# Performance work log

Hardware: AMD Instinct MI355X
Metric: run time of the kernel (lower is better)

Reference implementation:

```python
import jax, jax.numpy as jnp
import numpy as np

B, S, H, NH, FF, L = 2, 2048, 768, 12, 3072, 2
DH = H // NH
EPS = 1e-12
NEG = -10000.0


def setup_inputs() -> dict:
    key = jax.random.key(0)
    ks = jax.random.split(key, 10)
    w = lambda k, shp: jax.random.normal(k, shp, dtype=jnp.float32) * 0.02
    return {
        'hidden_states': jax.random.normal(ks[0], (B, S, H), dtype=jnp.float32),
        'attention_mask': jnp.ones((B, S), jnp.float32),
        'bias_matrix': jax.random.normal(ks[1], (S, S), dtype=jnp.float32) * 0.1,
        'bias_coef': jnp.ones((), jnp.float32),
        'Wq': w(ks[2], (L, H, H)), 'bq': jnp.zeros((L, H), jnp.float32),
        'Wk': w(ks[3], (L, H, H)), 'bk': jnp.zeros((L, H), jnp.float32),
        'Wv': w(ks[4], (L, H, H)), 'bv': jnp.zeros((L, H), jnp.float32),
        'Wo': w(ks[5], (L, H, H)), 'bo': jnp.zeros((L, H), jnp.float32),
        'ln1_g': jnp.ones((L, H), jnp.float32), 'ln1_b': jnp.zeros((L, H), jnp.float32),
        'Wi': w(ks[6], (L, H, FF)), 'bi': jnp.zeros((L, FF), jnp.float32),
        'Wo2': w(ks[7], (L, FF, H)), 'bo2': jnp.zeros((L, H), jnp.float32),
        'ln2_g': jnp.ones((L, H), jnp.float32), 'ln2_b': jnp.zeros((L, H), jnp.float32),
    }


def _layer_norm(x, g, b):
    mu = jnp.mean(x, axis=-1, keepdims=True)
    var = jnp.mean(jnp.square(x - mu), axis=-1, keepdims=True)
    return (x - mu) * jax.lax.rsqrt(var + EPS) * g + b


def reference(hidden_states, attention_mask, bias_matrix, bias_coef,
              Wq, bq, Wk, bk, Wv, bv, Wo, bo, ln1_g, ln1_b,
              Wi, bi, Wo2, bo2, ln2_g, ln2_b):
    # extended additive mask: [B,1,1,S]
    ext_mask = (1.0 - attention_mask)[:, None, None, :] * NEG
    bias = bias_matrix[None, None] * bias_coef  # [1,1,S,S]
    x = hidden_states
    scale = 1.0 / np.sqrt(DH)
    for i in range(L):
        q = (x @ Wq[i] + bq[i]).reshape(B, S, NH, DH).transpose(0, 2, 1, 3)
        k = (x @ Wk[i] + bk[i]).reshape(B, S, NH, DH).transpose(0, 2, 1, 3)
        v = (x @ Wv[i] + bv[i]).reshape(B, S, NH, DH).transpose(0, 2, 1, 3)
        scores = jnp.einsum('bhqd,bhkd->bhqk', q, k) * scale
        scores = scores + bias + ext_mask
        probs = jax.nn.softmax(scores, axis=-1)  # dropout = identity (eval)
        ctx = jnp.einsum('bhqk,bhkd->bhqd', probs, v)
        ctx = ctx.transpose(0, 2, 1, 3).reshape(B, S, H)
        attn_out = ctx @ Wo[i] + bo[i]
        x = _layer_norm(attn_out + x, ln1_g[i], ln1_b[i])
        inter = jax.nn.gelu(x @ Wi[i] + bi[i], approximate=False)
        ffn_out = inter @ Wo2[i] + bo2[i]
        x = _layer_norm(ffn_out + x, ln2_g[i], ln2_b[i])
    return x
```

## Files before the change

kernel.cpp:

```cpp
#include <hip/hip_runtime.h>
#include <hip/hip_bf16.h>
#include <math.h>

#define BB     2
#define SS     2048
#define HH     768
#define NHEAD  12
#define DHEAD  64
#define FFD    3072
#define NLAYER 2
#define MTOK   (BB*SS)
#define LOG2E  1.4426950408889634f
#define QSCALE 0.18033688011112042f

typedef __attribute__((ext_vector_type(8))) short bf16x8;
typedef __attribute__((ext_vector_type(4))) short bf16x4;
typedef __attribute__((ext_vector_type(4))) float f32x4;

__device__ __forceinline__ short f2bs(float f) {
    union { float f; unsigned u; } v; v.f = f;
    unsigned r = v.u + 0x7FFF + ((v.u >> 16) & 1);
    return (short)(r >> 16);
}
__device__ __forceinline__ float bs2f(short s) {
    union { unsigned u; float f; } v; v.u = ((unsigned)(unsigned short)s) << 16;
    return v.f;
}
__device__ __forceinline__ void gl2lds16(const short* g, short* l) {
    __builtin_amdgcn_global_load_lds(
        (const __attribute__((address_space(1))) unsigned int*)g,
        (__attribute__((address_space(3))) unsigned int*)l, 16, 0, 0);
}

struct TJobs { const float* src[8]; short* dst[8]; };

__global__ __launch_bounds__(256)
void transpose_cvt_batch(TJobs jobs, int K, int N)
{
    const float* __restrict__ W  = jobs.src[blockIdx.z];
    short* __restrict__ Wt = jobs.dst[blockIdx.z];
    __shared__ short tile[32][33];
    const int k0 = blockIdx.x * 32, n0 = blockIdx.y * 32;
    const int tx = threadIdx.x & 31, ty = threadIdx.x >> 5;
#pragma unroll
    for (int i = 0; i < 4; i++)
        tile[ty + i*8][tx] = f2bs(W[(size_t)(k0 + ty + i*8) * N + n0 + tx]);
    __syncthreads();
#pragma unroll
    for (int i = 0; i < 4; i++)
        Wt[(size_t)(n0 + ty + i*8) * K + k0 + tx] = tile[tx][ty + i*8];
}

__global__ __launch_bounds__(256)
void cvt_bf16(const float* __restrict__ src, short* __restrict__ dst, int n)
{
    const int i = blockIdx.x * 256 + threadIdx.x;
    if (i < n) dst[i] = f2bs(src[i]);
}

__global__ __launch_bounds__(256)
void pack_bias(const float* __restrict__ bq, const float* __restrict__ bk,
               const float* __restrict__ bv, float* __restrict__ bqkv)
{
    const int t = blockIdx.x * 256 + threadIdx.x;
    if (t >= NLAYER * 2304) return;
    const int l = t / 2304, r = t % 2304;
    const float* src = (r < 768) ? bq : (r < 1536 ? bk : bv);
    bqkv[t] = src[l*768 + (r % 768)];
}

__global__ __launch_bounds__(256)
void bias_frag_prep(const float* __restrict__ biasM, const float* __restrict__ mask,
                    const float* __restrict__ coefp, short* __restrict__ bFrag)
{
    __shared__ float tile[64][129];
    const int tid = threadIdx.x;
    const int qb = blockIdx.x, q0 = qb*64, k0 = blockIdx.y*128;
#pragma unroll
    for (int p = 0; p < 8; p++) {
        const int row = p*8 + (tid >> 5);
        const int col = (tid & 31) * 4;
        float4 v = *(const float4*)&biasM[(size_t)(q0 + row)*SS + k0 + col];
        tile[row][col+0] = v.x; tile[row][col+1] = v.y;
        tile[row][col+2] = v.z; tile[row][col+3] = v.w;
    }
    __syncthreads();
    const float coef = coefp[0];
    const int lane = tid & 63, w = tid >> 6;
    const int l16 = lane & 15, g = lane >> 4;
    const int qrow = w*16 + l16;
#pragma unroll
    for (int b = 0; b < BB; b++) {
#pragma unroll
        for (int kt = 0; kt < 8; kt++) {
            bf16x4 o;
#pragma unroll
            for (int r = 0; r < 4; r++) {
                const int kk = kt*16 + g*4 + r;
                const float madd = (1.f - mask[b*SS + k0 + kk]) * (-10000.0f);
                o[r] = f2bs((tile[qrow][kk] * coef + madd) * LOG2E);
            }
            const size_t idx = ((((size_t)b*32 + qb)*4 + w)*128 + (k0>>4) + kt)*256 + lane*4;
            *(bf16x4*)&bFrag[idx] = o;
        }
    }
}

__global__ __launch_bounds__(256)
void gemm_mfma(const short* __restrict__ A, const short* __restrict__ Bt,
               const float* __restrict__ bias, short* __restrict__ C, int ldc,
               int M, int N, int K, int gelu, short* __restrict__ VtOut, int vsplit,
               float qscale, int qcols)
{
    __shared__ short sA[2][128*32];
    __shared__ short sB[2][128*32];
    const int tid  = threadIdx.x;
    const int w    = tid >> 6;
    const int lane = tid & 63;
    const int l16  = lane & 15, g = lane >> 4;
    const int wm   = w & 1, wn = w >> 1;
    const size_t m0 = (size_t)blockIdx.y * 128, n0 = (size_t)blockIdx.x * 128;

    const int srow = lane >> 2;
    const int kc   = lane & 3;

    f32x4 acc[4][4];
#pragma unroll
    for (int i = 0; i < 4; i++)
#pragma unroll
        for (int j = 0; j < 4; j++) acc[i][j] = (f32x4){0.f,0.f,0.f,0.f};

    const short* gA0 = A  + (m0 + w*32 +      srow) * (size_t)K + kc*8;
    const short* gA1 = A  + (m0 + w*32 + 16 + srow) * (size_t)K + kc*8;
    const short* gB0 = Bt + (n0 + w*32 +      srow) * (size_t)K + kc*8;
    const short* gB1 = Bt + (n0 + w*32 + 16 + srow) * (size_t)K + kc*8;
    const int oA0 = (w*32     )*32, oA1 = (w*32 + 16)*32;

    for (int k0 = 0; k0 < K; k0 += 64) {
        gl2lds16(gA0 + k0,      &sA[0][oA0]);
        gl2lds16(gA1 + k0,      &sA[0][oA1]);
        gl2lds16(gB0 + k0,      &sB[0][oA0]);
        gl2lds16(gB1 + k0,      &sB[0][oA1]);
        gl2lds16(gA0 + k0 + 32, &sA[1][oA0]);
        gl2lds16(gA1 + k0 + 32, &sA[1][oA1]);
        gl2lds16(gB0 + k0 + 32, &sB[1][oA0]);
        gl2lds16(gB1 + k0 + 32, &sB[1][oA1]);
        __syncthreads();

#pragma unroll
        for (int s = 0; s < 2; s++) {
            bf16x8 af[4], bfr[4];
#pragma unroll
            for (int mt = 0; mt < 4; mt++)
                af[mt] = *(const bf16x8*)&sA[s][(wm*64 + mt*16 + l16)*32 + g*8];
#pragma unroll
            for (int nt = 0; nt < 4; nt++)
                bfr[nt] = *(const bf16x8*)&sB[s][(wn*64 + nt*16 + l16)*32 + g*8];
#pragma unroll
            for (int mt = 0; mt < 4; mt++)
#pragma unroll
                for (int nt = 0; nt < 4; nt++)
                    acc[mt][nt] = __builtin_amdgcn_mfma_f32_16x16x32_bf16(
                                      af[mt], bfr[nt], acc[mt][nt], 0, 0, 0);
        }
        __syncthreads();
    }

#pragma unroll
    for (int mt = 0; mt < 4; mt++) {
        const size_t row0 = m0 + wm*64 + mt*16 + g*4;
#pragma unroll
        for (int nt = 0; nt < 4; nt++) {
            const size_t col = n0 + wn*64 + nt*16 + l16;
            if ((int)col >= vsplit) {
                short4 t;
                t.x = f2bs(acc[mt][nt][0] + bias[col]);
                t.y = f2bs(acc[mt][nt][1] + bias[col]);
                t.z = f2bs(acc[mt][nt][2] + bias[col]);
                t.w = f2bs(acc[mt][nt][3] + bias[col]);
                *(short4*)&VtOut[(size_t)(col - vsplit)*MTOK + row0] = t;
            } else {
#pragma unroll
                for (int r = 0; r < 4; r++) {
                    float v = acc[mt][nt][r] + bias[col];
                    if ((int)col < qcols) v *= qscale;
                    if (gelu) v = 0.5f * v * (1.f + erff(v * 0.70710678118f));
                    C[(row0 + r) * (size_t)ldc + col] = f2bs(v);
                }
            }
        }
    }
}

__global__ __launch_bounds__(256)
void gemm_n64_splitk(const short* __restrict__ A, const short* __restrict__ Bt,
                     float* __restrict__ P, int K)
{
    const int K2 = K >> 1;
    const int z  = blockIdx.z;
    __shared__ short sA[2][128*32];
    __shared__ short sB[2][64*32];
    const int tid  = threadIdx.x;
    const int w    = tid >> 6;
    const int lane = tid & 63;
    const int l16  = lane & 15, g = lane >> 4;
    const int wm   = w & 1, wn = w >> 1;
    const size_t m0 = (size_t)blockIdx.y * 128, n0 = (size_t)blockIdx.x * 64;

    const int srow = lane >> 2;
    const int kc   = lane & 3;

    f32x4 acc[4][2];
#pragma unroll
    for (int i = 0; i < 4; i++)
#pragma unroll
        for (int j = 0; j < 2; j++) acc[i][j] = (f32x4){0.f,0.f,0.f,0.f};

    const short* gA0 = A  + (m0 + w*32 +      srow) * (size_t)K + z*K2 + kc*8;
    const short* gA1 = A  + (m0 + w*32 + 16 + srow) * (size_t)K + z*K2 + kc*8;
    const short* gB0 = Bt + (n0 + w*16 +      srow) * (size_t)K + z*K2 + kc*8;
    const int oA0 = (w*32     )*32, oA1 = (w*32 + 16)*32, oB0 = (w*16)*32;

    for (int k0 = 0; k0 < K2; k0 += 64) {
        gl2lds16(gA0 + k0,      &sA[0][oA0]);
        gl2lds16(gA1 + k0,      &sA[0][oA1]);
        gl2lds16(gB0 + k0,      &sB[0][oB0]);
        gl2lds16(gA0 + k0 + 32, &sA[1][oA0]);
        gl2lds16(gA1 + k0 + 32, &sA[1][oA1]);
        gl2lds16(gB0 + k0 + 32, &sB[1][oB0]);
        __syncthreads();

#pragma unroll
        for (int s = 0; s < 2; s++) {
            bf16x8 af[4], bfr[2];
#pragma unroll
            for (int mt = 0; mt < 4; mt++)
                af[mt] = *(const bf16x8*)&sA[s][(wm*64 + mt*16 + l16)*32 + g*8];
#pragma unroll
            for (int nt = 0; nt < 2; nt++)
                bfr[nt] = *(const bf16x8*)&sB[s][(wn*32 + nt*16 + l16)*32 + g*8];
#pragma unroll
            for (int mt = 0; mt < 4; mt++)
#pragma unroll
                for (int nt = 0; nt < 2; nt++)
                    acc[mt][nt] = __builtin_amdgcn_mfma_f32_16x16x32_bf16(
                                      af[mt], bfr[nt], acc[mt][nt], 0, 0, 0);
        }
        __syncthreads();
    }

    float* Pz = P + (size_t)z * MTOK * HH;
#pragma unroll
    for (int mt = 0; mt < 4; mt++) {
        const size_t row0 = m0 + wm*64 + mt*16 + g*4;
#pragma unroll
        for (int nt = 0; nt < 2; nt++) {
            const size_t col = n0 + wn*32 + nt*16 + l16;
#pragma unroll
            for (int r = 0; r < 4; r++)
                Pz[(row0 + r) * (size_t)HH + col] = acc[mt][nt][r];
        }
    }
}

__global__ __launch_bounds__(256, 3)
void attn_fused(const short* __restrict__ QK, const short* __restrict__ Vt,
                const short* __restrict__ bFrag, short* __restrict__ CTX)
{
    __shared__ short sK[128*72];
    __shared__ short sV[64*136];

    const int qb  = blockIdx.x;
    const int q0  = qb * 64;
    const int h   = blockIdx.y;
    const int b   = blockIdx.z;
    const int tid = threadIdx.x;
    const int w   = tid >> 6;
    const int lane = tid & 63;
    const int l16 = lane & 15;
    const int g   = lane >> 4;

    const short* qrow = QK + ((size_t)(b*SS) + q0 + w*16 + l16) * 1536 + h*64;
    bf16x8 bQ0 = *(const bf16x8*)(qrow + g*8);
    bf16x8 bQ1 = *(const bf16x8*)(qrow + 32 + g*8);

    f32x4 O[4];
#pragma unroll
    for (int d = 0; d < 4; d++) O[d] = (f32x4){0.f,0.f,0.f,0.f};
    float m_q = -1e30f, l_q = 0.f;

    const int krow = tid >> 3, kch = tid & 7;
    const int vrow = tid >> 4, vch = tid & 15;
    const short* Kg = QK + ((size_t)(b*SS) + krow)*1536 + 768 + h*64 + kch*8;
    const short* Vg = Vt + ((size_t)(h*64 + vrow))*MTOK + b*SS + vch*8;
    const short* bF = bFrag + ((((size_t)b*32 + qb)*4 + w)*128)*256 + lane*4;

    bf16x8 kreg[4], vreg[4];
#pragma unroll
    for (int p = 0; p < 4; p++) {
        kreg[p] = *(const bf16x8*)(Kg + (size_t)(p*32)*1536);
        vreg[p] = *(const bf16x8*)(Vg + (size_t)(p*16)*MTOK);
    }

    for (int k0 = 0; k0 < SS; k0 += 128) {
        const short* bFt = bF + ((size_t)(k0 >> 4))*256;
        bf16x4 bb[8];
#pragma unroll
        for (int t = 0; t < 8; t++)
            bb[t] = *(const bf16x4*)(bFt + (size_t)t*256);

#pragma unroll
        for (int p = 0; p < 4; p++) {
            *(bf16x8*)&sK[(p*32 + krow)*72 + kch*8]   = kreg[p];
            *(bf16x8*)&sV[(p*16 + vrow)*136 + vch*8]  = vreg[p];
        }
        __syncthreads();

        if (k0 + 128 < SS) {
#pragma unroll
            for (int p = 0; p < 4; p++) {
                kreg[p] = *(const bf16x8*)(Kg + (size_t)(k0 + 128 + p*32)*1536);
                vreg[p] = *(const bf16x8*)(Vg + (size_t)(p*16)*MTOK + k0 + 128);
            }
        }

        float S[8][4];
#pragma unroll
        for (int t = 0; t < 8; t++) {
            bf16x8 aK0 = *(const bf16x8*)&sK[(t*16 + l16)*72 + g*8];
            bf16x8 aK1 = *(const bf16x8*)&sK[(t*16 + l16)*72 + 32 + g*8];
            f32x4 c = (f32x4){0.f,0.f,0.f,0.f};
            c = __builtin_amdgcn_mfma_f32_16x16x32_bf16(aK0, bQ0, c, 0, 0, 0);
            c = __builtin_amdgcn_mfma_f32_16x16x32_bf16(aK1, bQ1, c, 0, 0, 0);
#pragma unroll
            for (int r = 0; r < 4; r++)
                S[t][r] = c[r] + bs2f(bb[t][r]);
        }

        float tm[8];
#pragma unroll
        for (int t = 0; t < 8; t++)
            tm[t] = fmaxf(fmaxf(S[t][0], S[t][1]), fmaxf(S[t][2], S[t][3]));
        float mx = fmaxf(fmaxf(fmaxf(tm[0], tm[1]), fmaxf(tm[2], tm[3])),
                         fmaxf(fmaxf(tm[4], tm[5]), fmaxf(tm[6], tm[7])));
        mx = fmaxf(mx, __shfl_xor(mx, 16));
        mx = fmaxf(mx, __shfl_xor(mx, 32));
        const float mnew  = fmaxf(m_q, mx);
        const float alpha = exp2f(m_q - mnew);
        float ts[8];
#pragma unroll
        for (int t = 0; t < 8; t++) {
            float p0 = exp2f(S[t][0] - mnew);
            float p1 = exp2f(S[t][1] - mnew);
            float p2 = exp2f(S[t][2] - mnew);
            float p3 = exp2f(S[t][3] - mnew);
            S[t][0] = p0; S[t][1] = p1; S[t][2] = p2; S[t][3] = p3;
            ts[t] = (p0 + p1) + (p2 + p3);
        }
        float rs = ((ts[0] + ts[1]) + (ts[2] + ts[3]))
                 + ((ts[4] + ts[5]) + (ts[6] + ts[7]));
        rs += __shfl_xor(rs, 16);
        rs += __shfl_xor(rs, 32);
        l_q = l_q * alpha + rs;
        m_q = mnew;

#pragma unroll
        for (int r = 0; r < 4; r++) {
            const float ar = __shfl(alpha, g*4 + r);
#pragma unroll
            for (int d = 0; d < 4; d++) O[d][r] *= ar;
        }

#define PVU(u)                                                                 \
        {                                                                      \
            unsigned pa, pb, pc, pe;                                           \
            asm("v_cvt_pk_bf16_f32 %0, %1, %2" : "=v"(pa)                      \
                : "v"(S[2*(u)][0]),   "v"(S[2*(u)][1]));                       \
            asm("v_cvt_pk_bf16_f32 %0, %1, %2" : "=v"(pb)                      \
                : "v"(S[2*(u)][2]),   "v"(S[2*(u)][3]));                       \
            asm("v_cvt_pk_bf16_f32 %0, %1, %2" : "=v"(pc)                      \
                : "v"(S[2*(u)+1][0]), "v"(S[2*(u)+1][1]));                     \
            asm("v_cvt_pk_bf16_f32 %0, %1, %2" : "=v"(pe)                      \
                : "v"(S[2*(u)+1][2]), "v"(S[2*(u)+1][3]));                     \
            asm("v_permlane32_swap_b32 %0, %1" : "+v"(pa), "+v"(pc));          \
            asm("v_permlane16_swap_b32 %0, %1" : "+v"(pa), "+v"(pc));          \
            asm("v_permlane32_swap_b32 %0, %1" : "+v"(pb), "+v"(pe));          \
            asm("v_permlane16_swap_b32 %0, %1" : "+v"(pb), "+v"(pe));          \
            union { unsigned uw[4]; bf16x8 v; } P_;                            \
            P_.uw[0] = pa; P_.uw[1] = pb; P_.uw[2] = pc; P_.uw[3] = pe;        \
            _Pragma("unroll")                                                  \
            for (int d = 0; d < 4; d++) {                                      \
                bf16x8 vv = *(const bf16x8*)&sV[(d*16 + l16)*136 + (u)*32 + g*8]; \
                O[d] = __builtin_amdgcn_mfma_f32_16x16x32_bf16(                \
                           P_.v, vv, O[d], 0, 0, 0);                           \
            }                                                                  \
        }
        PVU(0)
        PVU(1)
        PVU(2)
        PVU(3)
#undef PVU

        __syncthreads();
    }

    float linv[4];
#pragma unroll
    for (int r = 0; r < 4; r++)
        linv[r] = 1.f / __shfl(l_q, g*4 + r);
#pragma unroll
    for (int d = 0; d < 4; d++)
#pragma unroll
        for (int r = 0; r < 4; r++)
            CTX[((size_t)(b*SS) + q0 + w*16 + g*4 + r)*HH + h*64 + d*16 + l16]
                = f2bs(O[d][r] * linv[r]);
}

__global__ __launch_bounds__(256)
void add_ln3(const float* __restrict__ P, const float* __restrict__ bvec,
             const short* __restrict__ R,
             const float* __restrict__ g, const float* __restrict__ beta,
             short* __restrict__ Out, float* __restrict__ OutF)
{
    const int lane = threadIdx.x & 63;
    const int row  = blockIdx.x * 4 + (threadIdx.x >> 6);
    const size_t base = (size_t)row * HH;
    const size_t sH = (size_t)MTOK * HH;

    float v[12];
    float s = 0.f;
#pragma unroll
    for (int p = 0; p < 3; p++) {
        const int c = p*256 + lane*4;
        float4 p0 = *(const float4*)&P[base + c];
        float4 p1 = *(const float4*)&P[sH + base + c];
        float4 bv4 = *(const float4*)&bvec[c];
        bf16x4 rv = *(const bf16x4*)&R[base + c];
        float x0 = p0.x + p1.x + bv4.x + bs2f(rv[0]);
        float x1 = p0.y + p1.y + bv4.y + bs2f(rv[1]);
        float x2 = p0.z + p1.z + bv4.z + bs2f(rv[2]);
        float x3 = p0.w + p1.w + bv4.w + bs2f(rv[3]);
        v[p*4+0] = x0; v[p*4+1] = x1; v[p*4+2] = x2; v[p*4+3] = x3;
        s += (x0 + x1) + (x2 + x3);
    }
    s += __shfl_xor(s, 1);  s += __shfl_xor(s, 2);  s += __shfl_xor(s, 4);
    s += __shfl_xor(s, 8);  s += __shfl_xor(s, 16); s += __shfl_xor(s, 32);
    const float mu = s * (1.f / HH);

    float s2 = 0.f;
#pragma unroll
    for (int j = 0; j < 12; j++) { float d = v[j] - mu; s2 += d * d; }
    s2 += __shfl_xor(s2, 1);  s2 += __shfl_xor(s2, 2);  s2 += __shfl_xor(s2, 4);
    s2 += __shfl_xor(s2, 8);  s2 += __shfl_xor(s2, 16); s2 += __shfl_xor(s2, 32);
    const float rstd = rsqrtf(s2 * (1.f / HH) + 1e-12f);

#pragma unroll
    for (int p = 0; p < 3; p++) {
        const int c = p*256 + lane*4;
        float4 gv = *(const float4*)&g[c];
        float4 bv = *(const float4*)&beta[c];
        float o0 = (v[p*4+0] - mu) * rstd * gv.x + bv.x;
        float o1 = (v[p*4+1] - mu) * rstd * gv.y + bv.y;
        float o2 = (v[p*4+2] - mu) * rstd * gv.z + bv.z;
        float o3 = (v[p*4+3] - mu) * rstd * gv.w + bv.w;
        bf16x4 ov; ov[0] = f2bs(o0); ov[1] = f2bs(o1); ov[2] = f2bs(o2); ov[3] = f2bs(o3);
        *(bf16x4*)&Out[base + c] = ov;
        if (OutF) {
            float4 of; of.x = o0; of.y = o1; of.z = o2; of.w = o3;
            *(float4*)&OutF[base + c] = of;
        }
    }
}

extern "C" void kernel_launch(void* const* d_in, const int* in_sizes, int n_in,
                              void* d_out, int out_size, void* d_ws, size_t ws_size,
                              hipStream_t stream)
{
    const float* hs    = (const float*)d_in[0];
    const float* mask  = (const float*)d_in[1];
    const float* biasM = (const float*)d_in[2];
    const float* coef  = (const float*)d_in[3];
    const float* Wq    = (const float*)d_in[4];
    const float* bq    = (const float*)d_in[5];
    const float* Wk    = (const float*)d_in[6];
    const float* bk    = (const float*)d_in[7];
    const float* Wv    = (const float*)d_in[8];
    const float* bv    = (const float*)d_in[9];
    const float* Wo    = (const float*)d_in[10];
    const float* bo    = (const float*)d_in[11];
    const float* ln1g  = (const float*)d_in[12];
    const float* ln1b  = (const float*)d_in[13];
    const float* Wi    = (const float*)d_in[14];
    const float* bi    = (const float*)d_in[15];
    const float* Wo2   = (const float*)d_in[16];
    const float* bo2   = (const float*)d_in[17];
    const float* ln2g  = (const float*)d_in[18];
    const float* ln2b  = (const float*)d_in[19];

    const size_t sH   = (size_t)MTOK * HH;
    const size_t sQK  = (size_t)MTOK * 1536;
    const size_t sVt  = (size_t)HH * MTOK;
    const size_t WPL  = 7077888;
    short* wt    = (short*)d_ws;
    float* bqkv  = (float*)(wt + 2*WPL);
    short* bFrag = (short*)(bqkv + 2*2304);
    short* X     = bFrag + (size_t)2*SS*SS;
    short* X2    = X  + sH;
    short* QK    = X2 + sH;
    short* Vt    = QK + sQK;
    short* CTX   = Vt + sVt;
    float* PK    = (float*)(CTX + sH);
    short* INTER = QK;

    const dim3 blk(256);

    TJobs jH, jI, jO;
    for (int l = 0; l < NLAYER; l++) {
        short* wl = wt + (size_t)l * WPL;
        jH.src[l*4+0] = Wq + (size_t)l*HH*HH;  jH.dst[l*4+0] = wl;
        jH.src[l*4+1] = Wk + (size_t)l*HH*HH;  jH.dst[l*4+1] = wl + 768*768;
        jH.src[l*4+2] = Wv + (size_t)l*HH*HH;  jH.dst[l*4+2] = wl + 1536*768;
        jH.src[l*4+3] = Wo + (size_t)l*HH*HH;  jH.dst[l*4+3] = wl + 1769472;
        jI.src[l] = Wi  + (size_t)l*HH*FFD;    jI.dst[l] = wl + 2359296;
        jO.src[l] = Wo2 + (size_t)l*FFD*HH;    jO.dst[l] = wl + 4718592;
    }
    transpose_cvt_batch<<<dim3(24,24,8), blk, 0, stream>>>(jH, HH, HH);
    transpose_cvt_batch<<<dim3(24,96,2), blk, 0, stream>>>(jI, HH, FFD);
    transpose_cvt_batch<<<dim3(96,24,2), blk, 0, stream>>>(jO, FFD, HH);
    bias_frag_prep<<<dim3(SS/64, SS/128), blk, 0, stream>>>(biasM, mask, coef, bFrag);
    pack_bias<<<dim3((NLAYER*2304 + 255)/256), blk, 0, stream>>>(bq, bk, bv, bqkv);
    cvt_bf16<<<dim3((int)((sH + 255)/256)), blk, 0, stream>>>(hs, X, (int)sH);

    const dim3 gQKV(2304/128, MTOK/128);
    const dim3 gSK (HH/64,    MTOK/128, 2);
    const dim3 gFF (FFD/128,  MTOK/128);
    const dim3 gA  (SS/64, NHEAD, BB);
    const dim3 gLN (MTOK/4);
    const int NOSPLIT = 1 << 30;

    for (int l = 0; l < NLAYER; l++) {
        short* wl = wt + (size_t)l * WPL;
        gemm_mfma<<<gQKV, blk, 0, stream>>>(X, wl, bqkv + l*2304, QK, 1536,
                                            MTOK, 2304, HH, 0, Vt, 1536,
                                            QSCALE, 768);
        attn_fused<<<gA, blk, 0, stream>>>(QK, Vt, bFrag, CTX);
        gemm_n64_splitk<<<gSK, blk, 0, stream>>>(CTX, wl + 1769472, PK, HH);
        add_ln3<<<gLN, blk, 0, stream>>>(PK, bo + l*HH, X, ln1g + l*HH, ln1b + l*HH,
                                         X2, nullptr);
        gemm_mfma<<<gFF, blk, 0, stream>>>(X2, wl + 2359296, bi + l*FFD, INTER, FFD,
                                           MTOK, FFD, HH, 1, nullptr, NOSPLIT,
                                           1.f, 0);
        gemm_n64_splitk<<<gSK, blk, 0, stream>>>(INTER, wl + 4718592, PK, FFD);
        add_ln3<<<gLN, blk, 0, stream>>>(PK, bo2 + l*HH, X2, ln2g + l*HH, ln2b + l*HH,
                                         X, (l == NLAYER-1) ? (float*)d_out : nullptr);
    }
}
```

Before: 569.8 us.

## Double-buffer K in LDS, load V fragments straight to registers, use raw v_exp

The attention kernel now keeps two K tiles in LDS so the next tile is written while the current one is consumed, leaving one barrier per iteration. V fragments are no longer staged through LDS: each lane loads its MFMA operand directly from global memory in two halves, ping-ponged so the loads overlap the PV matmuls. exp2f is replaced with the raw v_exp_f32 instruction to drop range-handling code. The aim is less LDS traffic, fewer barriers and better latency hiding, at the cost of more VGPRs (16 extra bf16x8 registers), which could reduce occupancy under launch_bounds(256,3). Global V reads also become less coalesced.

```diff
diff --git a/kernel.cpp b/kernel.cpp
--- a/kernel.cpp
+++ b/kernel.cpp
@@ -26,6 +26,9 @@
     union { unsigned u; float f; } v; v.u = ((unsigned)(unsigned short)s) << 16;
     return v.f;
 }
+__device__ __forceinline__ float fexp2(float x) {
+    float r; asm("v_exp_f32 %0, %1" : "=v"(r) : "v"(x)); return r;
+}
 __device__ __forceinline__ void gl2lds16(const short* g, short* l) {
     __builtin_amdgcn_global_load_lds(
         (const __attribute__((address_space(1))) unsigned int*)g,
@@ -267,8 +270,7 @@
 void attn_fused(const short* __restrict__ QK, const short* __restrict__ Vt,
                 const short* __restrict__ bFrag, short* __restrict__ CTX)
 {
-    __shared__ short sK[128*72];
-    __shared__ short sV[64*136];
+    __shared__ short sK[2][128*72];
 
     const int qb  = blockIdx.x;
     const int q0  = qb * 64;
@@ -290,45 +292,42 @@
     float m_q = -1e30f, l_q = 0.f;
 
     const int krow = tid >> 3, kch = tid & 7;
-    const int vrow = tid >> 4, vch = tid & 15;
     const short* Kg = QK + ((size_t)(b*SS) + krow)*1536 + 768 + h*64 + kch*8;
-    const short* Vg = Vt + ((size_t)(h*64 + vrow))*MTOK + b*SS + vch*8;
+    const short* Vg = Vt + ((size_t)(h*64 + l16))*MTOK + b*SS + g*8;
     const short* bF = bFrag + ((((size_t)b*32 + qb)*4 + w)*128)*256 + lane*4;
 
-    bf16x8 kreg[4], vreg[4];
-#pragma unroll
-    for (int p = 0; p < 4; p++) {
+    bf16x8 kreg[4], vfA[8], vfB[8];
+#pragma unroll
+    for (int p = 0; p < 4; p++)
         kreg[p] = *(const bf16x8*)(Kg + (size_t)(p*32)*1536);
-        vreg[p] = *(const bf16x8*)(Vg + (size_t)(p*16)*MTOK);
-    }
+#pragma unroll
+    for (int p = 0; p < 4; p++)
+        *(bf16x8*)&sK[0][(p*32 + krow)*72 + kch*8] = kreg[p];
+#pragma unroll
+    for (int p = 0; p < 4; p++)
+        kreg[p] = *(const bf16x8*)(Kg + (size_t)(128 + p*32)*1536);
+#pragma unroll
+    for (int u = 0; u < 2; u++)
+#pragma unroll
+        for (int d = 0; d < 4; d++)
+            vfA[u*4+d] = *(const bf16x8*)(Vg + (size_t)(d*16)*MTOK + u*32);
+    __syncthreads();
 
     for (int k0 = 0; k0 < SS; k0 += 128) {
+        const int cur = (k0 >> 7) & 1;
+        const short* sKc = sK[cur];
+
         const short* bFt = bF + ((size_t)(k0 >> 4))*256;
         bf16x4 bb[8];
 #pragma unroll
         for (int t = 0; t < 8; t++)
             bb[t] = *(const bf16x4*)(bFt + (size_t)t*256);
 
-#pragma unroll
-        for (int p = 0; p < 4; p++) {
-            *(bf16x8*)&sK[(p*32 + krow)*72 + kch*8]   = kreg[p];
-            *(bf16x8*)&sV[(p*16 + vrow)*136 + vch*8]  = vreg[p];
-        }
-        __syncthreads();
-
-        if (k0 + 128 < SS) {
-#pragma unroll
-            for (int p = 0; p < 4; p++) {
-                kreg[p] = *(const bf16x8*)(Kg + (size_t)(k0 + 128 + p*32)*1536);
-                vreg[p] = *(const bf16x8*)(Vg + (size_t)(p*16)*MTOK + k0 + 128);
-            }
-        }
-
         float S[8][4];
 #pragma unroll
         for (int t = 0; t < 8; t++) {
-            bf16x8 aK0 = *(const bf16x8*)&sK[(t*16 + l16)*72 + g*8];
-            bf16x8 aK1 = *(const bf16x8*)&sK[(t*16 + l16)*72 + 32 + g*8];
+            bf16x8 aK0 = *(const bf16x8*)&sKc[(t*16 + l16)*72 + g*8];
+            bf16x8 aK1 = *(const bf16x8*)&sKc[(t*16 + l16)*72 + 32 + g*8];
             f32x4 c = (f32x4){0.f,0.f,0.f,0.f};
             c = __builtin_amdgcn_mfma_f32_16x16x32_bf16(aK0, bQ0, c, 0, 0, 0);
             c = __builtin_amdgcn_mfma_f32_16x16x32_bf16(aK1, bQ1, c, 0, 0, 0);
@@ -336,6 +335,24 @@
             for (int r = 0; r < 4; r++)
                 S[t][r] = c[r] + bs2f(bb[t][r]);
         }
+
+        if (k0 + 128 < SS) {
+            short* sKn = sK[cur ^ 1];
+#pragma unroll
+            for (int p = 0; p < 4; p++)
+                *(bf16x8*)&sKn[(p*32 + krow)*72 + kch*8] = kreg[p];
+            if (k0 + 256 < SS) {
+#pragma unroll
+                for (int p = 0; p < 4; p++)
+                    kreg[p] = *(const bf16x8*)(Kg + (size_t)(k0 + 256 + p*32)*1536);
+            }
+        }
+
+#pragma unroll
+        for (int u = 0; u < 2; u++)
+#pragma unroll
+            for (int d = 0; d < 4; d++)
+                vfB[u*4+d] = *(const bf16x8*)(Vg + (size_t)(d*16)*MTOK + k0 + 64 + u*32);
 
         float tm[8];
 #pragma unroll
@@ -346,14 +363,14 @@
         mx = fmaxf(mx, __shfl_xor(mx, 16));
         mx = fmaxf(mx, __shfl_xor(mx, 32));
         const float mnew  = fmaxf(m_q, mx);
-        const float alpha = exp2f(m_q - mnew);
+        const float alpha = fexp2(m_q - mnew);
         float ts[8];
 #pragma unroll
         for (int t = 0; t < 8; t++) {
-            float p0 = exp2f(S[t][0] - mnew);
-            float p1 = exp2f(S[t][1] - mnew);
-            float p2 = exp2f(S[t][2] - mnew);
-            float p3 = exp2f(S[t][3] - mnew);
+            float p0 = fexp2(S[t][0] - mnew);
+            float p1 = fexp2(S[t][1] - mnew);
+            float p2 = fexp2(S[t][2] - mnew);
+            float p3 = fexp2(S[t][3] - mnew);
             S[t][0] = p0; S[t][1] = p1; S[t][2] = p2; S[t][3] = p3;
             ts[t] = (p0 + p1) + (p2 + p3);
         }
@@ -371,7 +388,7 @@
             for (int d = 0; d < 4; d++) O[d][r] *= ar;
         }
 
-#define PVU(u)                                                                 \
+#define PVU(u, vh)                                                             \
         {                                                                      \
             unsigned pa, pb, pc, pe;                                           \
             asm("v_cvt_pk_bf16_f32 %0, %1, %2" : "=v"(pa)                      \
@@ -389,16 +406,23 @@
             union { unsigned uw[4]; bf16x8 v; } P_;                            \
             P_.uw[0] = pa; P_.uw[1] = pb; P_.uw[2] = pc; P_.uw[3] = pe;        \
             _Pragma("unroll")                                                  \
-            for (int d = 0; d < 4; d++) {                                      \
-                bf16x8 vv = *(const bf16x8*)&sV[(d*16 + l16)*136 + (u)*32 + g*8]; \
+            for (int d = 0; d < 4; d++)                                        \
                 O[d] = __builtin_amdgcn_mfma_f32_16x16x32_bf16(                \
-                           P_.v, vv, O[d], 0, 0, 0);                           \
-            }                                                                  \
-        }
-        PVU(0)
-        PVU(1)
-        PVU(2)
-        PVU(3)
+                           P_.v, vh[((u)&1)*4 + d], O[d], 0, 0, 0);            \
+        }
+        PVU(0, vfA)
+        PVU(1, vfA)
+
+        if (k0 + 128 < SS) {
+#pragma unroll
+            for (int u = 0; u < 2; u++)
+#pragma unroll
+                for (int d = 0; d < 4; d++)
+                    vfA[u*4+d] = *(const bf16x8*)(Vg + (size_t)(d*16)*MTOK + k0 + 128 + u*32);
+        }
+
+        PVU(2, vfB)
+        PVU(3, vfB)
 #undef PVU
 
         __syncthreads();
```

Result: slower. 661.0 us (+16.0%).
